# Kernel optimization log

Hardware: AMD Instinct MI355X
Metric: run time of the kernel (lower is better)

## Reference

```python
import jax, jax.numpy as jnp
import numpy as np
from jax import lax

B, L, D, H, V = 512, 60, 300, 256, 50000
NEG_INF = 10000.0  # the TF code uses -10000.0 as -inf in the mask


def setup_inputs() -> dict:
    key = jax.random.key(0)
    ks = jax.random.split(key, 18)
    s = 0.05
    rn = lambda k, shape: jax.random.normal(k, shape, jnp.float32) * s
    return {
        "E": rn(ks[0], (V, D)),
        "Wx1": rn(ks[1], (D, 4 * H)), "Wh1": rn(ks[2], (H, 4 * H)), "b1": jnp.zeros((4 * H,), jnp.float32),
        "Wx2": rn(ks[3], (D, 4 * H)), "Wh2": rn(ks[4], (H, 4 * H)), "b2": jnp.zeros((4 * H,), jnp.float32),
        "W_y": rn(ks[5], (H, H)), "Wh_a": rn(ks[6], (H, H)), "Wr_a": rn(ks[7], (H, H)),
        "w_a": rn(ks[8], (H,)), "Wt_a": rn(ks[9], (H, H)), "Wp_a": rn(ks[10], (H, H)), "Wxa": rn(ks[11], (H, H)),
        "U": rn(ks[12], (H, 2)), "b_out": jnp.zeros((1, 2), jnp.float32),
        "input1": jax.random.randint(ks[13], (B, L), 0, V, jnp.int32),
        "input2": jax.random.randint(ks[14], (B, L), 0, V, jnp.int32),
        "seqlen1": jax.random.randint(ks[15], (B,), 1, L + 1, jnp.int32),
        "seqlen2": jax.random.randint(ks[16], (B,), 1, L + 1, jnp.int32),
    }


def lstm_scan(x, seqlen, Wx, Wh, b):
    # TF BasicLSTMCell (forget_bias=1.0, gate order i,j,f,o) with dynamic_rnn
    # sequence_length semantics: past seqlen, output is 0 and state is frozen.
    Bsz = x.shape[0]
    h0 = jnp.zeros((Bsz, Wh.shape[0]), x.dtype)
    # precompute input projection for all timesteps: [L, B, 4H]
    xg = jnp.einsum('bld,dk->lbk', x, Wx) + b

    def step(carry, inputs):
        c, h = carry
        g_t, t = inputs
        gates = g_t + h @ Wh
        i, j, f, o = jnp.split(gates, 4, axis=-1)
        c_new = c * jax.nn.sigmoid(f + 1.0) + jax.nn.sigmoid(i) * jnp.tanh(j)
        h_new = jnp.tanh(c_new) * jax.nn.sigmoid(o)
        m = (t < seqlen)[:, None]
        return (jnp.where(m, c_new, c), jnp.where(m, h_new, h)), jnp.where(m, h_new, 0.0)

    (_, h_last), Y = lax.scan(step, (h0, h0), (xg, jnp.arange(x.shape[1])))
    return jnp.transpose(Y, (1, 0, 2)), h_last  # Y: [B, L, H]


def reference(E, Wx1, Wh1, b1, Wx2, Wh2, b2, W_y, Wh_a, Wr_a, w_a, Wt_a, Wp_a, Wxa,
              U, b_out, input1, input2, seqlen1, seqlen2):
    def mask_for(s):
        return jnp.where(jnp.arange(L)[None, :] < s[:, None], 0.0, -NEG_INF).astype(jnp.float32)

    def attend(Y, Y2, last_h, s2, mask1):
        # word-by-word attention (score_type=1 path):
        # M_t = tanh(W_y Y + (W_h h_t + W_r r_{t-1})), alpha_t = softmax(w.M_t + mask)
        # r_t = Y alpha_t + tanh(W_t r_{t-1})
        WyY = jnp.einsum('blh,hk->blk', Y, W_y)  # [B, L, H]
        r0 = jnp.zeros_like(last_h)

        def step(r, h_t):
            tmp = h_t @ Wh_a + r @ Wr_a                      # [B, H]
            M = jnp.tanh(WyY + tmp[:, None, :])              # [B, L, H]
            alpha = jax.nn.softmax(jnp.einsum('blh,h->bl', M, w_a) + mask1, axis=1)
            r_new = jnp.einsum('bl,blh->bh', alpha, Y) + jnp.tanh(r @ Wt_a)
            return r_new, r_new

        _, rs = lax.scan(step, r0, jnp.transpose(Y2, (1, 0, 2)))  # rs: [L, B, H]
        oh = jax.nn.one_hot(s2 - 1, L, dtype=Y.dtype)             # select r at last valid step
        r_L = jnp.einsum('bl,lbh->bh', oh, rs)
        return jnp.tanh(r_L @ Wp_a + last_h @ Wxa)

    def branch(tok1, tok2, s1, s2):
        x1, x2 = E[tok1], E[tok2]
        Y, _ = lstm_scan(x1, s1, Wx1, Wh1, b1)
        Y2, h2 = lstm_scan(x2, s2, Wx2, Wh2, b2)
        return attend(Y, Y2, h2, s2, mask_for(s1))

    last_h = branch(input1, input2, seqlen1, seqlen2) + branch(input2, input1, seqlen2, seqlen1)
    # dropout keep_prob = 1.0 (inference) -> identity
    return last_h @ U + b_out  # [B, 2]
```

## Files before the change

### kernel.cpp

```cpp
#include <hip/hip_runtime.h>
#include <cstdint>
#include <cstddef>

#define B_  512
#define L_  60
#define D_  300
#define H_  256
#define BT  1024
#define KX  320
#define KL  576
#define NG  1024
#define NBLK 512

typedef _Float16 half8   __attribute__((ext_vector_type(8)));
typedef _Float16 half4_t __attribute__((ext_vector_type(4)));
typedef float    floatx4 __attribute__((ext_vector_type(4)));

__device__ __forceinline__ float fast_tanh(float x){
    float e = __expf(2.f*x);
    return 1.f - 2.f*__builtin_amdgcn_rcpf(e + 1.f);
}
__device__ __forceinline__ float sigm(float x){
    return __builtin_amdgcn_rcpf(1.f + __expf(-x));
}

#define MFMA16(a,b,c) __builtin_amdgcn_mfma_f32_16x16x32_f16(a,b,c,0,0,0)

__global__ void k_fill4(uint4* __restrict__ p, int n4, uint32_t v){
    uint4 q = {v, v, v, v};
    int i = blockIdx.x*blockDim.x + threadIdx.x;
    int st = gridDim.x*blockDim.x;
    for (; i < n4; i += st) p[i] = q;
}

__global__ void k_sched(const int* __restrict__ s1, const int* __restrict__ s2,
                        int* __restrict__ perm)
{
    __shared__ int bins[61];
    __shared__ int base[61];
    const int tid = threadIdx.x;
    if (tid < 61) bins[tid] = 0;
    __syncthreads();
    int cap = (tid < B_) ? s2[tid] : s1[tid - B_];
    atomicAdd(&bins[cap], 1);
    __syncthreads();
    if (tid == 0) {
        int acc = 0;
        for (int c = 60; c >= 1; --c) { base[c] = acc; acc += bins[c]; }
    }
    __syncthreads();
    int pos = atomicAdd(&base[cap], 1);
    perm[pos] = tid;
}

__global__ __launch_bounds__(256, 2) void k_prep(
    const float* __restrict__ E,
    const float* __restrict__ Wx1, const float* __restrict__ Wh1,
    const float* __restrict__ Wx2, const float* __restrict__ Wh2,
    const float* __restrict__ W_y, const float* __restrict__ Wh_a, const float* __restrict__ Wr_a,
    const float* __restrict__ Wt_a, const float* __restrict__ Wp_a, const float* __restrict__ Wxa,
    const int* __restrict__ in1, const int* __restrict__ in2,
    _Float16* __restrict__ X16, _Float16* __restrict__ BcatT, _Float16* __restrict__ AW)
{
    const int tid = threadIdx.x;
    const int bid = blockIdx.x;

    for (int it = 0; it < 19; ++it) {
        int gid = it*131072 + bid*256 + tid;
        if (gid < 2457600) {
            int row = gid / (L_*40);
            int rem = gid - row*(L_*40);
            int t  = rem / 40;
            int ch = rem - t*40;
            int k0 = ch*8;
            int tok = (row < B_) ? in1[row*L_ + t] : in2[(row - B_)*L_ + t];
            const float* src = E + (size_t)tok*D_ + k0;
            half8 o;
            #pragma unroll
            for (int k = 0; k < 8; ++k) o[k] = (_Float16)0.f;
            if (k0 + 8 <= D_) {
                float4 a = *(const float4*)(src);
                float4 b = *(const float4*)(src + 4);
                o[0]=(_Float16)a.x; o[1]=(_Float16)a.y; o[2]=(_Float16)a.z; o[3]=(_Float16)a.w;
                o[4]=(_Float16)b.x; o[5]=(_Float16)b.y; o[6]=(_Float16)b.z; o[7]=(_Float16)b.w;
            } else if (k0 < D_) {
                float4 a = *(const float4*)(src);
                o[0]=(_Float16)a.x; o[1]=(_Float16)a.y; o[2]=(_Float16)a.z; o[3]=(_Float16)a.w;
            }
            *(half8*)(X16 + ((size_t)row*L_ + t)*KX + k0) = o;
        }
    }
    for (int it = 0; it < 9; ++it) {
        int idx = it*131072 + bid*256 + tid;
        int set = (idx >= KL*NG) ? 1 : 0;
        int rem = idx - set*(KL*NG);
        int k = rem >> 10, n = rem & 1023;
        const float* Wx = set ? Wx2 : Wx1;
        const float* Wh = set ? Wh2 : Wh1;
        float v = 0.f;
        if (k < D_)       v = Wx[k*NG + n];
        else if (k >= KX) v = Wh[(k - KX)*NG + n];
        BcatT[((size_t)set*NG + n)*KL + k] = (_Float16)v;
    }
    for (int it = 0; it < 4; ++it) {
        int idx = it*131072 + bid*256 + tid;
        if (idx < 458752) {
            float v; int dst;
            if (idx < 65536) {
                int k = idx >> 8, n = idx & 255;
                v = W_y[k*256 + n];
                dst = n*256 + k;
            } else if (idx < 131072) {
                int j = idx - 65536; int k = j >> 8, n = j & 255;
                v = Wh_a[k*256 + n];
                dst = 65536 + n*256 + k;
            } else if (idx < 262144) {
                int j = idx - 131072; int n = j >> 8, k = j & 255;
                v = (n < 256) ? Wr_a[k*256 + n] : Wt_a[k*256 + (n - 256)];
                dst = 131072 + n*256 + k;
            } else {
                int j = idx - 262144; int n = j >> 9, k = j & 511;
                v = (k < 256) ? Wp_a[k*256 + n] : Wxa[(k - 256)*256 + n];
                dst = 262144 + n*512 + k;
            }
            AW[dst] = (_Float16)v;
        }
    }
}

__global__ __launch_bounds__(256, 2) void k_lstm(
    const float* __restrict__ b1, const float* __restrict__ b2,
    const int* __restrict__ s1, const int* __restrict__ s2,
    const _Float16* __restrict__ X16, _Float16* __restrict__ Y16,
    const _Float16* __restrict__ BcatT,
    unsigned long long* __restrict__ hT, _Float16* __restrict__ hfin)
{
    __shared__ __align__(16) unsigned char shm[33792];

    const int tid = threadIdx.x;
    const int bid = blockIdx.x;
    const int lane = tid & 63, wv = tid >> 6;
    const int q = lane >> 4, lm = lane & 15;

    float (*sG)[64][65] = (float(*)[64][65])shm;
    _Float16* sA = (_Float16*)shm;

    const int ht = bid & 15, mt = bid >> 4;
    const int set = mt >> 4;
    const int m0 = mt*64;
    const int kh = wv >> 1;
    const int wn = (wv & 1)*32;
    const int cb = wn >> 4;

    half8 bfr[9][2];
    #pragma unroll
    for (int ch = 0; ch < 9; ++ch)
        #pragma unroll
        for (int ti = 0; ti < 2; ++ti) {
            bfr[ch][ti] = *(const half8*)(BcatT +
                ((size_t)set*NG + (cb+ti)*256 + ht*16 + lm)*KL + kh*288 + ch*32 + q*8);
            asm volatile("" : "+v"(bfr[ch][ti]));
        }

    const int amA = tid >> 2, kgA = (tid & 3)*8;
    const int pairA = kgA >> 1;
    const int rsA = (m0 + amA) & 1023;
    const int xrowA = set ? ((rsA + 512) & 1023) : rsA;

    const float* bias = set ? b2 : b1;
    const int pc = tid & 7;
    const int eh = ht*16 + pc*2;
    float bI[2], bJ[2], bF[2], bO[2];
    #pragma unroll
    for (int j = 0; j < 2; ++j) {
        bI[j] = bias[eh + j]; bJ[j] = bias[256 + eh + j];
        bF[j] = bias[512 + eh + j]; bO[j] = bias[768 + eh + j];
    }
    int esl[2]; float c_st[2][2], h_st[2][2];
    #pragma unroll
    for (int rp = 0; rp < 2; ++rp) {
        int rs = (m0 + (tid >> 3) + rp*32) & 1023;
        esl[rp] = (set == 0) ? ((rs < B_) ? s1[rs] : s2[rs - B_])
                             : ((rs < B_) ? s2[rs] : s1[rs - B_]);
        c_st[rp][0] = 0.f; c_st[rp][1] = 0.f;
        h_st[rp][0] = 0.f; h_st[rp][1] = 0.f;
    }

    half8 zero8;
    #pragma unroll
    for (int k = 0; k < 8; ++k) zero8[k] = (_Float16)0.f;

    for (int t = 0; t < L_; ++t) {
        const _Float16* aX = X16 + ((size_t)xrowA*L_ + t)*KX;
        const unsigned long long* hbase =
            hT + ((size_t)(((t - 1) & 1)*2 + set)*BT + rsA)*128;
        unsigned long long* hTo = hT + (size_t)((t & 1)*2 + set)*BT*128;
        const uint32_t wantTag = (uint32_t)(t - 1);

        floatx4 acc[4][2];
        #pragma unroll
        for (int mi = 0; mi < 4; ++mi)
            #pragma unroll
            for (int ti = 0; ti < 2; ++ti) acc[mi][ti] = (floatx4){0.f,0.f,0.f,0.f};

        half8 av0 = *(const half8*)(aX + kgA);
        half8 av1 = *(const half8*)(aX + 288 + kgA);
        unsigned long long hw[4];

        #pragma unroll
        for (int i = 0; i < 9; ++i) {
            __syncthreads();
            if (i > 0) {
                if (t > 0) {
                    const unsigned long long* hb = hbase + (i - 1)*16 + pairA;
                    #pragma unroll
                    for (int k = 0; k < 4; ++k) {
                        unsigned long long w = hw[k];
                        while ((uint32_t)(w >> 32) != wantTag)
                            w = __hip_atomic_load(hb + k, __ATOMIC_RELAXED,
                                                  __HIP_MEMORY_SCOPE_AGENT);
                        hw[k] = w;
                    }
                    union { uint32_t u[4]; half8 v; } cv;
                    #pragma unroll
                    for (int k = 0; k < 4; ++k) cv.u[k] = (uint32_t)hw[k];
                    av1 = cv.v;
                } else {
                    av1 = zero8;
                }
            }
            *(half8*)(sA + (     amA)*40 + kgA) = av0;
            *(half8*)(sA + (64 + amA)*40 + kgA) = av1;
            __syncthreads();
            if (i < 8) {
                av0 = *(const half8*)(aX + (i + 1)*32 + kgA);
                if (t > 0) {
                    const unsigned long long* hb = hbase + i*16 + pairA;
                    #pragma unroll
                    for (int k = 0; k < 4; ++k)
                        hw[k] = __hip_atomic_load(hb + k, __ATOMIC_RELAXED,
                                                  __HIP_MEMORY_SCOPE_AGENT);
                }
            }
            half8 af[4];
            #pragma unroll
            for (int mi = 0; mi < 4; ++mi)
                af[mi] = *(const half8*)(sA + (kh*64 + mi*16 + lm)*40 + q*8);
            #pragma unroll
            for (int mi = 0; mi < 4; ++mi) {
                acc[mi][0] = MFMA16(af[mi], bfr[i][0], acc[mi][0]);
                acc[mi][1] = MFMA16(af[mi], bfr[i][1], acc[mi][1]);
            }
        }

        __syncthreads();
        #pragma unroll
        for (int mi = 0; mi < 4; ++mi)
            #pragma unroll
            for (int ti = 0; ti < 2; ++ti)
                #pragma unroll
                for (int r = 0; r < 4; ++r)
                    sG[kh][mi*16 + q*4 + r][wn + ti*16 + lm] = acc[mi][ti][r];
        __syncthreads();

        #pragma unroll
        for (int rp = 0; rp < 2; ++rp) {
            int row = (tid >> 3) + rp*32;
            int gr = m0 + row;
            int rs = gr & 1023;
            bool act = (t < esl[rp]);
            union { _Float16 h[2]; uint32_t u; } hp, yp;
            #pragma unroll
            for (int j = 0; j < 2; ++j) {
                int hh = pc*2 + j;
                float gi = sG[0][row][     hh] + sG[1][row][     hh] + bI[j];
                float gj = sG[0][row][16 + hh] + sG[1][row][16 + hh] + bJ[j];
                float gf = sG[0][row][32 + hh] + sG[1][row][32 + hh] + bF[j];
                float go = sG[0][row][48 + hh] + sG[1][row][48 + hh] + bO[j];
                float c_new = c_st[rp][j]*sigm(gf + 1.f) + sigm(gi)*fast_tanh(gj);
                float h_new = fast_tanh(c_new)*sigm(go);
                if (act) { c_st[rp][j] = c_new; h_st[rp][j] = h_new; }
                hp.h[j] = (_Float16)h_st[rp][j];
                yp.h[j] = act ? (_Float16)h_new : (_Float16)0.f;
            }
            unsigned long long w = ((unsigned long long)(uint32_t)t << 32)
                                 | (unsigned long long)hp.u;
            __hip_atomic_store(hTo + (size_t)rs*128 + (eh >> 1), w,
                               __ATOMIC_RELAXED, __HIP_MEMORY_SCOPE_AGENT);
            if (set == 1 && t == L_ - 1)
                *(uint32_t*)(hfin + (size_t)rs*H_ + eh) = hp.u;
            *(uint32_t*)(Y16 + ((size_t)gr*L_ + t)*H_ + eh) = yp.u;
        }
    }
}

__global__ __launch_bounds__(256, 2) void k_wyth(
    const _Float16* __restrict__ Y16, _Float16* __restrict__ WyY16,
    _Float16* __restrict__ TH16, const _Float16* __restrict__ AW)
{
    __shared__ __align__(16) _Float16 sB[64*264];

    const int tid = threadIdx.x;
    const int bid = blockIdx.x;
    const int lane = tid & 63, wv = tid >> 6;
    const int q = lane >> 4, lm = lane & 15;

    const int slot = bid & 7;
    const int z = slot >> 2, nt = slot & 3;
    const int n0 = nt*64;
    {
        int rowB = tid >> 2;
        int kb = (tid & 3)*64;
        #pragma unroll
        for (int s = 0; s < 8; ++s)
            *(half8*)(sB + rowB*264 + kb + s*8) =
                *(const half8*)(AW + (size_t)z*65536 + (size_t)(n0 + rowB)*H_ + kb + s*8);
    }
    __syncthreads();
    const _Float16* Ybase = Y16 + (size_t)z*((size_t)BT*L_*H_);
    _Float16* dst = z ? TH16 : WyY16;
    for (int mi_ = 0; mi_ < 15; ++mi_) {
        int m0w = ((bid >> 3) + mi_*64)*64;
        floatx4 acc[4];
        #pragma unroll
        for (int ti = 0; ti < 4; ++ti) acc[ti] = (floatx4){0.f,0.f,0.f,0.f};
        const _Float16* aRow = Ybase + (size_t)(m0w + wv*16 + lm)*H_ + q*8;
        #pragma unroll
        for (int ch = 0; ch < 8; ++ch) {
            half8 a = *(const half8*)(aRow + ch*32);
            #pragma unroll
            for (int ti = 0; ti < 4; ++ti) {
                half8 b = *(const half8*)(sB + (ti*16 + lm)*264 + ch*32 + q*8);
                acc[ti] = MFMA16(a, b, acc[ti]);
            }
        }
        #pragma unroll
        for (int ti = 0; ti < 4; ++ti)
            #pragma unroll
            for (int r = 0; r < 4; ++r)
                dst[(size_t)(m0w + wv*16 + q*4 + r)*H_ + n0 + ti*16 + lm] = (_Float16)acc[ti][r];
    }
}

__global__ __launch_bounds__(512, 2) void k_att(
    const float* __restrict__ w_a, const int* __restrict__ s1, const int* __restrict__ s2,
    const _Float16* __restrict__ Y16, const _Float16* __restrict__ WyY16,
    const _Float16* __restrict__ TH16, const _Float16* __restrict__ AW,
    const int* __restrict__ perm, _Float16* __restrict__ rL16)
{
    __shared__ __align__(16) unsigned char shm[141056];

    _Float16* sY  = (_Float16*)shm;
    _Float16* sWy = (_Float16*)(shm + 61440);
    _Float16* sR  = (_Float16*)(shm + 124800);
    float*    sTW = (float*)(shm + 133248);
    float*    sWt = (float*)(shm + 135360);
    float*    sLog= (float*)(shm + 137408);
    float*    sAl = (float*)(shm + 137920);
    float*    sWa = (float*)(shm + 139968);
    int*      sU  = (int*)(shm + 140992);
    int*      sCap= (int*)(shm + 141000);
    int*      sAtt= (int*)(shm + 141008);

    const int tid = threadIdx.x;
    const int wv = tid >> 6, lane = tid & 63;
    const int q = lane >> 4, lm = lane & 15;

    if (tid < 2) {
        int u = perm[blockIdx.x*2 + tid];
        sU[tid] = u;
        sCap[tid] = (u < B_) ? s2[u] : s1[u - B_];
        sAtt[tid] = (u < B_) ? s1[u] : s2[u - B_];
    }
    __syncthreads();
    const int uA = sU[0], uB = sU[1];

    if (tid < 256) sWa[tid] = w_a[tid];
    for (int i = tid; i < 16*264; i += 512) sR[i] = (_Float16)0.f;
    for (int i = tid; i < 2*60*32; i += 512) {
        int row = i / 1920;
        int rem = i - row*1920;
        int l = rem >> 5, ch = rem & 31;
        int u = row ? uB : uA;
        *(half8*)(sY  + row*15360 + l*256 + ch*8) =
            *(const half8*)(Y16   + ((size_t)u*L_ + l)*H_ + ch*8);
        *(half8*)(sWy + row*15840 + l*264 + ch*8) =
            *(const half8*)(WyY16 + ((size_t)u*L_ + l)*H_ + ch*8);
    }
    half8 bfr[4][8];
    const _Float16* WrtT = AW + 131072;
    #pragma unroll
    for (int ti = 0; ti < 4; ++ti)
        #pragma unroll
        for (int ch = 0; ch < 8; ++ch) {
            bfr[ti][ch] = *(const half8*)(WrtT + (size_t)((wv*4 + ti)*16 + lm)*256 + ch*32 + q*8);
            asm volatile("" : "+v"(bfr[ti][ch]));
        }
    __syncthreads();

    const int cap0 = sCap[0], cap1 = sCap[1];
    const int att0 = sAtt[0], att1 = sAtt[1];
    const int mcap = max(cap0, cap1);

    const int rowB = wv >> 2, sB_ = wv & 3;
    const int lsub = lane >> 2, li = lane & 3;
    const int saB = rowB ? att1 : att0;
    const int rowD = tid >> 8, hD = tid & 255;
    const int capD = rowD ? cap1 : cap0;
    const int saD  = rowD ? att1 : att0;
    const int uD   = rowD ? uB : uA;

    const bool thl = (wv < 4) && (q == 0);
    const int  tc0 = (wv*4+0)*16 + lm, tc1 = (wv*4+1)*16 + lm,
               tc2 = (wv*4+2)*16 + lm, tc3 = (wv*4+3)*16 + lm;
    const _Float16* tb0 = TH16 + (size_t)uA*L_*H_;
    const _Float16* tb1 = TH16 + (size_t)uB*L_*H_;
    _Float16 thn[8];
    #pragma unroll
    for (int k = 0; k < 8; ++k) thn[k] = (_Float16)0.f;
    if (thl) {
        thn[0] = tb0[tc0]; thn[1] = tb0[tc1]; thn[2] = tb0[tc2]; thn[3] = tb0[tc3];
        thn[4] = tb1[tc0]; thn[5] = tb1[tc1]; thn[6] = tb1[tc2]; thn[7] = tb1[tc3];
    }

    for (int t = 0; t < mcap; ++t) {
        _Float16 thc[8];
        #pragma unroll
        for (int k = 0; k < 8; ++k) thc[k] = thn[k];
        if (thl && (t + 1 < mcap)) {
            const size_t o = (size_t)(t + 1)*H_;
            thn[0] = tb0[o + tc0]; thn[1] = tb0[o + tc1];
            thn[2] = tb0[o + tc2]; thn[3] = tb0[o + tc3];
            thn[4] = tb1[o + tc0]; thn[5] = tb1[o + tc1];
            thn[6] = tb1[o + tc2]; thn[7] = tb1[o + tc3];
        }
        floatx4 acc[4];
        #pragma unroll
        for (int ti = 0; ti < 4; ++ti) acc[ti] = (floatx4){0.f,0.f,0.f,0.f};
        #pragma unroll
        for (int ch = 0; ch < 8; ++ch) {
            half8 a = *(const half8*)(sR + lm*264 + ch*32 + q*8);
            #pragma unroll
            for (int ti = 0; ti < 4; ++ti)
                acc[ti] = MFMA16(a, bfr[ti][ch], acc[ti]);
        }
        if (q == 0) {
            if (wv < 4) {
                #pragma unroll
                for (int ti = 0; ti < 4; ++ti) {
                    int col = (wv*4 + ti)*16 + lm;
                    sTW[col]       = acc[ti][0] + (float)thc[ti];
                    sTW[264 + col] = acc[ti][1] + (float)thc[4 + ti];
                }
            } else {
                #pragma unroll
                for (int ti = 0; ti < 4; ++ti) {
                    int col = (wv*4 + ti)*16 + lm - 256;
                    sWt[col]       = fast_tanh(acc[ti][0]);
                    sWt[256 + col] = fast_tanh(acc[ti][1]);
                }
            }
        }
        __syncthreads();

        {
            int l = sB_*16 + lsub;
            float v = 0.f;
            if (l < saB) {
                const _Float16* wy = sWy + rowB*15840 + l*264;
                const float* tw = sTW + rowB*264;
                #pragma unroll
                for (int j = 0; j < 16; ++j) {
                    int h0 = j*16 + li*4;
                    half4_t yv = *(const half4_t*)(wy + h0);
                    #pragma unroll
                    for (int k = 0; k < 4; ++k)
                        v += fast_tanh((float)yv[k] + tw[h0 + k]) * sWa[h0 + k];
                }
            }
            v += __shfl_xor(v, 1);
            v += __shfl_xor(v, 2);
            if (li == 0 && l < saB) sLog[rowB*64 + l] = v;
        }
        __syncthreads();

        {
            float x = (lane < saB) ? sLog[rowB*64 + lane] : -3.4e38f;
            float m = x;
            #pragma unroll
            for (int off = 32; off > 0; off >>= 1) m = fmaxf(m, __shfl_xor(m, off));
            float e = (lane < saB) ? __expf(x - m) : 0.f;
            float ssum = e;
            #pragma unroll
            for (int off = 32; off > 0; off >>= 1) ssum += __shfl_xor(ssum, off);
            sAl[wv*64 + lane] = e * __builtin_amdgcn_rcpf(ssum);
        }

        if (t < capD) {
            const _Float16* yb = sY + rowD*15360 + hD;
            const float* al = sAl + wv*64;
            float a0 = 0.f, a1 = 0.f, a2 = 0.f, a3 = 0.f;
            int l = 0;
            for (; l + 4 <= saD; l += 4) {
                a0 += al[l]     * (float)yb[(size_t)l*256];
                a1 += al[l + 1] * (float)yb[(size_t)(l + 1)*256];
                a2 += al[l + 2] * (float)yb[(size_t)(l + 2)*256];
                a3 += al[l + 3] * (float)yb[(size_t)(l + 3)*256];
            }
            for (; l < saD; ++l) a0 += al[l] * (float)yb[(size_t)l*256];
            float rv = ((a0 + a1) + (a2 + a3)) + sWt[rowD*256 + hD];
            sR[rowD*264 + hD] = (_Float16)rv;
            if (t == capD - 1)
                rL16[(size_t)uD*H_ + hD] = (_Float16)rv;
        }
        __syncthreads();
    }
}

__global__ __launch_bounds__(256, 2) void k_ff(
    const _Float16* __restrict__ rL16, const _Float16* __restrict__ hfin,
    const _Float16* __restrict__ AW, float* __restrict__ ff)
{
    __shared__ __align__(16) unsigned char shm[10240];

    const int tid = threadIdx.x;
    const int bid = blockIdx.x;
    const int lane = tid & 63, wv = tid >> 6;
    const int q = lane >> 4, lm = lane & 15;

    _Float16* sA = (_Float16*)shm;
    _Float16* sB = (_Float16*)(shm + 5120);
    const _Float16* WfinT = AW + 262144;
    const int n0 = (bid & 3)*64, m0 = (bid >> 2)*64;
    const int wm = (wv & 1)*32, wn = (wv >> 1)*32;
    const int am = tid >> 2, kg = (tid & 3)*8;
    const int row = m0 + am;
    const _Float16* bRow = WfinT + (size_t)(n0 + am)*512;
    floatx4 acc00 = {0.f,0.f,0.f,0.f}, acc01 = acc00, acc10 = acc00, acc11 = acc00;
    for (int ch = 0; ch < 16; ++ch) {
        const int k0 = ch*32;
        half8 av = (k0 < 256) ? *(const half8*)(rL16 + (size_t)row*H_ + k0 + kg)
                              : *(const half8*)(hfin + (size_t)row*H_ + (k0 - 256) + kg);
        half8 bv = *(const half8*)(bRow + k0 + kg);
        __syncthreads();
        *(half8*)(sA + am*40 + kg) = av;
        *(half8*)(sB + am*40 + kg) = bv;
        __syncthreads();
        half8 a0v = *(const half8*)(sA + (wm + lm)*40 + q*8);
        half8 a1v = *(const half8*)(sA + (wm + 16 + lm)*40 + q*8);
        half8 b0v = *(const half8*)(sB + (wn + lm)*40 + q*8);
        half8 b1v = *(const half8*)(sB + (wn + 16 + lm)*40 + q*8);
        acc00 = MFMA16(a0v, b0v, acc00); acc01 = MFMA16(a0v, b1v, acc01);
        acc10 = MFMA16(a1v, b0v, acc10); acc11 = MFMA16(a1v, b1v, acc11);
    }
    int rb = m0 + wm + q*4, col = n0 + wn + lm;
    #pragma unroll
    for (int r = 0; r < 4; ++r) {
        ff[(size_t)(rb + r)*H_ + col]           = acc00[r];
        ff[(size_t)(rb + r)*H_ + col + 16]      = acc01[r];
        ff[(size_t)(rb + 16 + r)*H_ + col]      = acc10[r];
        ff[(size_t)(rb + 16 + r)*H_ + col + 16] = acc11[r];
    }
}

__global__ __launch_bounds__(256, 2) void k_out(
    const float* __restrict__ U, const float* __restrict__ b_o,
    const float* __restrict__ ff, float* __restrict__ out)
{
    __shared__ __align__(16) unsigned char shm[18432];

    const int tid = threadIdx.x;
    const int bid = blockIdx.x;
    const int lane = tid & 63, wv = tid >> 6;

    float* sTh = (float*)shm;
    float* sU  = (float*)(shm + 16384);
    const int b0 = bid*16;
    sU[tid] = U[tid]; sU[256 + tid] = U[256 + tid];
    for (int idx = tid; idx < 16*256; idx += 256) {
        int r = idx >> 8, h = idx & 255;
        sTh[idx] = fast_tanh(ff[(size_t)(b0 + r)*256 + h]) + fast_tanh(ff[(size_t)(b0 + r + 512)*256 + h]);
    }
    __syncthreads();
    for (int r = wv; r < 16; r += 4) {
        float p0 = 0.f, p1 = 0.f;
        #pragma unroll
        for (int k = 0; k < 4; ++k) {
            int h = lane*4 + k;
            float v = sTh[r*256 + h];
            p0 += v * sU[h*2];
            p1 += v * sU[h*2 + 1];
        }
        #pragma unroll
        for (int off = 32; off > 0; off >>= 1) { p0 += __shfl_down(p0, off); p1 += __shfl_down(p1, off); }
        if (lane == 0) {
            out[(b0 + r)*2]     = p0 + b_o[0];
            out[(b0 + r)*2 + 1] = p1 + b_o[1];
        }
    }
}

extern "C" void kernel_launch(void* const* d_in, const int* in_sizes, int n_in,
                              void* d_out, int out_size, void* d_ws, size_t ws_size,
                              hipStream_t stream)
{
    (void)in_sizes; (void)n_in; (void)out_size; (void)ws_size;
    const float* E    = (const float*)d_in[0];
    const float* Wx1  = (const float*)d_in[1];
    const float* Wh1  = (const float*)d_in[2];
    const float* b1   = (const float*)d_in[3];
    const float* Wx2  = (const float*)d_in[4];
    const float* Wh2  = (const float*)d_in[5];
    const float* b2   = (const float*)d_in[6];
    const float* W_y  = (const float*)d_in[7];
    const float* Wh_a = (const float*)d_in[8];
    const float* Wr_a = (const float*)d_in[9];
    const float* w_a  = (const float*)d_in[10];
    const float* Wt_a = (const float*)d_in[11];
    const float* Wp_a = (const float*)d_in[12];
    const float* Wxa  = (const float*)d_in[13];
    const float* U    = (const float*)d_in[14];
    const float* b_o  = (const float*)d_in[15];
    const int* in1 = (const int*)d_in[16];
    const int* in2 = (const int*)d_in[17];
    const int* s1  = (const int*)d_in[18];
    const int* s2  = (const int*)d_in[19];
    float* out = (float*)d_out;

    char* p = (char*)d_ws;
    auto alloc = [&](size_t bytes) { char* r = p; p += (bytes + 255) & ~(size_t)255; return r; };
    _Float16* X16   = (_Float16*)alloc((size_t)BT*L_*KX*2);
    _Float16* Y16   = (_Float16*)alloc(2ull*BT*L_*H_*2);
    _Float16* WyY16 = (_Float16*)alloc((size_t)BT*L_*H_*2);
    _Float16* TH16  = (_Float16*)alloc((size_t)BT*L_*H_*2);
    _Float16* BcatT = (_Float16*)alloc(2ull*NG*KL*2);
    _Float16* AW    = (_Float16*)alloc(393216ull*2);
    unsigned long long* hT = (unsigned long long*)alloc(4ull*BT*128*8);
    _Float16* hfin  = (_Float16*)alloc((size_t)BT*H_*2);
    _Float16* rL16  = (_Float16*)alloc((size_t)BT*H_*2);
    float*    ff    = (float*)   alloc((size_t)BT*H_*4);
    int*      perm  = (int*)     alloc(4096);

    k_fill4<<<256, 256, 0, stream>>>((uint4*)hT, (int)(4ull*BT*128*8/16), 0xFFFFFFFFu);
    k_sched<<<1, 1024, 0, stream>>>(s1, s2, perm);
    k_prep<<<NBLK, 256, 0, stream>>>(E, Wx1, Wh1, Wx2, Wh2,
        W_y, Wh_a, Wr_a, Wt_a, Wp_a, Wxa, in1, in2, X16, BcatT, AW);
    k_lstm<<<NBLK, 256, 0, stream>>>(b1, b2, s1, s2, X16, Y16, BcatT, hT, hfin);
    k_wyth<<<NBLK, 256, 0, stream>>>(Y16, WyY16, TH16, AW);
    k_att<<<512, 512, 0, stream>>>(w_a, s1, s2, Y16, WyY16, TH16, AW, perm, rL16);
    k_ff<<<64, 256, 0, stream>>>(rL16, hfin, AW, ff);
    k_out<<<32, 256, 0, stream>>>(U, b_o, ff, out);
}
```

Measured before the change: 1.084 ms.

## Fuse WyY projection into attention kernel, computed from shared-memory Y tile

The W_y*Y projection is no longer computed by k_wyth and written to a global WyY16 buffer. Instead, each attention block computes it with MFMA from the Y rows already staged in shared memory and writes the result directly into sWy. k_wyth now only produces the TH projection. This removes a global write and read of a full B*L*H fp16 tensor, at the cost of extra MFMA work and a sync inside k_att, with W_y read from global per block.

```diff
diff --git a/kernel.cpp b/kernel.cpp
--- a/kernel.cpp
+++ b/kernel.cpp
@@ -295,8 +295,8 @@
 }
 
 __global__ __launch_bounds__(256, 2) void k_wyth(
-    const _Float16* __restrict__ Y16, _Float16* __restrict__ WyY16,
-    _Float16* __restrict__ TH16, const _Float16* __restrict__ AW)
+    const _Float16* __restrict__ Y16, _Float16* __restrict__ TH16,
+    const _Float16* __restrict__ AW)
 {
     __shared__ __align__(16) _Float16 sB[64*264];
 
@@ -305,8 +305,7 @@
     const int lane = tid & 63, wv = tid >> 6;
     const int q = lane >> 4, lm = lane & 15;
 
-    const int slot = bid & 7;
-    const int z = slot >> 2, nt = slot & 3;
+    const int nt = bid & 3;
     const int n0 = nt*64;
     {
         int rowB = tid >> 2;
@@ -314,13 +313,14 @@
         #pragma unroll
         for (int s = 0; s < 8; ++s)
             *(half8*)(sB + rowB*264 + kb + s*8) =
-                *(const half8*)(AW + (size_t)z*65536 + (size_t)(n0 + rowB)*H_ + kb + s*8);
-    }
-    __syncthreads();
-    const _Float16* Ybase = Y16 + (size_t)z*((size_t)BT*L_*H_);
-    _Float16* dst = z ? TH16 : WyY16;
-    for (int mi_ = 0; mi_ < 15; ++mi_) {
-        int m0w = ((bid >> 3) + mi_*64)*64;
+                *(const half8*)(AW + 65536 + (size_t)(n0 + rowB)*H_ + kb + s*8);
+    }
+    __syncthreads();
+    const _Float16* Ybase = Y16 + (size_t)BT*L_*H_;
+    for (int it = 0; it < 8; ++it) {
+        int m = (bid >> 2) + it*128;
+        if (m >= 960) break;
+        int m0w = m*64;
         floatx4 acc[4];
         #pragma unroll
         for (int ti = 0; ti < 4; ++ti) acc[ti] = (floatx4){0.f,0.f,0.f,0.f};
@@ -338,15 +338,15 @@
         for (int ti = 0; ti < 4; ++ti)
             #pragma unroll
             for (int r = 0; r < 4; ++r)
-                dst[(size_t)(m0w + wv*16 + q*4 + r)*H_ + n0 + ti*16 + lm] = (_Float16)acc[ti][r];
+                TH16[(size_t)(m0w + wv*16 + q*4 + r)*H_ + n0 + ti*16 + lm] = (_Float16)acc[ti][r];
     }
 }
 
 __global__ __launch_bounds__(512, 2) void k_att(
     const float* __restrict__ w_a, const int* __restrict__ s1, const int* __restrict__ s2,
-    const _Float16* __restrict__ Y16, const _Float16* __restrict__ WyY16,
-    const _Float16* __restrict__ TH16, const _Float16* __restrict__ AW,
-    const int* __restrict__ perm, _Float16* __restrict__ rL16)
+    const _Float16* __restrict__ Y16, const _Float16* __restrict__ TH16,
+    const _Float16* __restrict__ AW, const int* __restrict__ perm,
+    _Float16* __restrict__ rL16)
 {
     __shared__ __align__(16) unsigned char shm[141056];
 
@@ -382,11 +382,33 @@
         int rem = i - row*1920;
         int l = rem >> 5, ch = rem & 31;
         int u = row ? uB : uA;
-        *(half8*)(sY  + row*15360 + l*256 + ch*8) =
-            *(const half8*)(Y16   + ((size_t)u*L_ + l)*H_ + ch*8);
-        *(half8*)(sWy + row*15840 + l*264 + ch*8) =
-            *(const half8*)(WyY16 + ((size_t)u*L_ + l)*H_ + ch*8);
-    }
+        *(half8*)(sY + row*15360 + l*256 + ch*8) =
+            *(const half8*)(Y16 + ((size_t)u*L_ + l)*H_ + ch*8);
+    }
+    __syncthreads();
+
+    {
+        const _Float16* WyT = AW;
+        const int rrb = wv*16;
+        for (int nt2 = 0; nt2 < 16; ++nt2) {
+            floatx4 a4 = (floatx4){0.f,0.f,0.f,0.f};
+            #pragma unroll
+            for (int ch = 0; ch < 8; ++ch) {
+                int rr = rrb + lm;
+                half8 a = *(const half8*)(sY + (rr >> 6)*15360 + (rr & 63)*256 + ch*32 + q*8);
+                half8 b = *(const half8*)(WyT + (size_t)(nt2*16 + lm)*256 + ch*32 + q*8);
+                a4 = MFMA16(a, b, a4);
+            }
+            #pragma unroll
+            for (int r = 0; r < 4; ++r) {
+                int rr2 = rrb + q*4 + r;
+                int l2 = rr2 & 63;
+                if (l2 < 60)
+                    sWy[(rr2 >> 6)*15840 + l2*264 + nt2*16 + lm] = (_Float16)a4[r];
+            }
+        }
+    }
+
     half8 bfr[4][8];
     const _Float16* WrtT = AW + 131072;
     #pragma unroll
@@ -631,7 +653,6 @@
     auto alloc = [&](size_t bytes) { char* r = p; p += (bytes + 255) & ~(size_t)255; return r; };
     _Float16* X16   = (_Float16*)alloc((size_t)BT*L_*KX*2);
     _Float16* Y16   = (_Float16*)alloc(2ull*BT*L_*H_*2);
-    _Float16* WyY16 = (_Float16*)alloc((size_t)BT*L_*H_*2);
     _Float16* TH16  = (_Float16*)alloc((size_t)BT*L_*H_*2);
     _Float16* BcatT = (_Float16*)alloc(2ull*NG*KL*2);
     _Float16* AW    = (_Float16*)alloc(393216ull*2);
@@ -646,8 +667,8 @@
     k_prep<<<NBLK, 256, 0, stream>>>(E, Wx1, Wh1, Wx2, Wh2,
         W_y, Wh_a, Wr_a, Wt_a, Wp_a, Wxa, in1, in2, X16, BcatT, AW);
     k_lstm<<<NBLK, 256, 0, stream>>>(b1, b2, s1, s2, X16, Y16, BcatT, hT, hfin);
-    k_wyth<<<NBLK, 256, 0, stream>>>(Y16, WyY16, TH16, AW);
-    k_att<<<512, 512, 0, stream>>>(w_a, s1, s2, Y16, WyY16, TH16, AW, perm, rL16);
+    k_wyth<<<NBLK, 256, 0, stream>>>(Y16, TH16, AW);
+    k_att<<<512, 512, 0, stream>>>(w_a, s1, s2, Y16, TH16, AW, perm, rL16);
     k_ff<<<64, 256, 0, stream>>>(rL16, hfin, AW, ff);
     k_out<<<32, 256, 0, stream>>>(U, b_o, ff, out);
 }
```

After: 1.122 ms. 3.5% more time.
